# Performance work log

Measured on AMD Instinct MI355X. Metric: run time of the kernel, lower is better.

The kernel has to match this reference:

```python
import jax, jax.numpy as jnp
import numpy as np
from jax import lax

WINDOW = 11
SIGMA = 1.5
K1 = 0.01
K2 = 0.03
DATA_RANGE = 1.0


def _gaussian_kernel(channels):
    coords = jnp.arange(WINDOW, dtype=jnp.float32) - (WINDOW // 2)
    g = jnp.exp(-(coords ** 2) / (2.0 * SIGMA ** 2))
    g = g / g.sum()
    k2d = g[:, None] * g[None, :]                      # [W, W]
    # depthwise kernel, OIHW with I=1, O=channels (feature_group_count=channels)
    return jnp.broadcast_to(k2d, (channels, 1, WINDOW, WINDOW))


def _depthwise_blur(img, kernel, channels):
    pad = WINDOW // 2
    return lax.conv_general_dilated(
        img, kernel,
        window_strides=(1, 1),
        padding=[(pad, pad), (pad, pad)],
        dimension_numbers=('NCHW', 'OIHW', 'NCHW'),
        feature_group_count=channels,
    )


def setup_inputs() -> dict:
    key = jax.random.key(0)
    kx, ky = jax.random.split(key)
    shape = (16, 3, 512, 512)
    x = jax.random.uniform(kx, shape, dtype=jnp.float32)
    y = jax.random.uniform(ky, shape, dtype=jnp.float32)
    return {"x": x, "y": y}


def reference(x, y):
    channels = x.shape[1]
    kernel = _gaussian_kernel(channels)

    mu_x = _depthwise_blur(x, kernel, channels)
    mu_y = _depthwise_blur(y, kernel, channels)
    mu_x_sq = mu_x * mu_x
    mu_y_sq = mu_y * mu_y
    mu_xy = mu_x * mu_y

    sigma_x_sq = _depthwise_blur(x * x, kernel, channels) - mu_x_sq
    sigma_y_sq = _depthwise_blur(y * y, kernel, channels) - mu_y_sq
    sigma_xy = _depthwise_blur(x * y, kernel, channels) - mu_xy

    C1 = (K1 * DATA_RANGE) ** 2
    C2 = (K2 * DATA_RANGE) ** 2
    numerator = (2.0 * mu_xy + C1) * (2.0 * sigma_xy + C2)
    denominator = (mu_x_sq + mu_y_sq + C1) * (sigma_x_sq + sigma_y_sq + C2)
    ssim_map = numerator / (denominator + 1e-8)
    return 1.0 - ssim_map.mean()
```

## Files before the change

kernel.cpp:

```cpp
#include <hip/hip_runtime.h>
#include <cmath>

#define WIN 11
#define HALO 5
#define IMG 512
#define NIMG 48
#define TS 64
#define HR (TS + 2*HALO)
#define NTILE (IMG/TS)
#define NBLK (NIMG*NTILE*NTILE)
#define NPIX (16.0 * 3.0 * 512.0 * 512.0)

typedef _Float16 f16;
typedef _Float16 h2 __attribute__((ext_vector_type(2)));

struct GaussW { float w[WIN]; };

__device__ __forceinline__ unsigned pk2(float a, float b) {
    auto h = __builtin_amdgcn_cvt_pkrtz(a, b);
    return __builtin_bit_cast(unsigned, h);
}
__device__ __forceinline__ h2 uph(unsigned u) {
    return __builtin_bit_cast(h2, u);
}

__global__ void __launch_bounds__(64) zero_kernel(float* out) {
    if (threadIdx.x == 0) out[0] = 0.f;
}

__global__ void __launch_bounds__(64) finish_kernel(float* out) {
    if (threadIdx.x == 0)
        out[0] = 1.0f - out[0] * (float)(1.0 / NPIX);
}

template<int USE_ATOMIC>
__global__ void __launch_bounds__(256) fused_ssim(
        const float* __restrict__ xin, const float* __restrict__ yin,
        float* __restrict__ outp, GaussW W) {
    __shared__ uint4 hb[HR][32];
    __shared__ float wsum[4];
    const int tid = threadIdx.x;
    const int tx = blockIdx.x, ty = blockIdx.y;
    const size_t ibase = (size_t)blockIdx.z * (size_t)(IMG * IMG);
    const float* __restrict__ xb = xin + ibase;
    const float* __restrict__ yb = yin + ibase;

    const int cg  = tid & 15;
    const int rr  = tid >> 4;
    const int gx0 = tx * TS + cg * 4 - HALO;
    const bool cint = (gx0 >= 0) && (gx0 + 13 < IMG);

    #pragma unroll
    for (int it = 0; it < 5; ++it) {
        const int r = it * 16 + rr;
        if (r < HR) {
            const int gy = ty * TS - HALO + r;
            if ((unsigned)gy < IMG) {
                const float* xr = xb + (size_t)gy * IMG;
                const float* yr = yb + (size_t)gy * IMG;
                float xv[14], yv[14];
                if (cint) {
                    xv[0] = xr[gx0];  yv[0] = yr[gx0];
                    #pragma unroll
                    for (int q = 0; q < 3; ++q) {
                        float4 a = *(const float4*)(xr + gx0 + 1 + 4*q);
                        float4 b = *(const float4*)(yr + gx0 + 1 + 4*q);
                        xv[1+4*q]=a.x; xv[2+4*q]=a.y; xv[3+4*q]=a.z; xv[4+4*q]=a.w;
                        yv[1+4*q]=b.x; yv[2+4*q]=b.y; yv[3+4*q]=b.z; yv[4+4*q]=b.w;
                    }
                    xv[13] = xr[gx0 + 13];  yv[13] = yr[gx0 + 13];
                } else {
                    #pragma unroll
                    for (int j = 0; j < 14; ++j) {
                        int gx = gx0 + j;
                        bool ok = ((unsigned)gx < IMG);
                        xv[j] = ok ? xr[gx] : 0.f;
                        yv[j] = ok ? yr[gx] : 0.f;
                    }
                }
                float ax[4]  = {0,0,0,0}, ay[4]  = {0,0,0,0};
                float as_[4] = {0,0,0,0}, axy[4] = {0,0,0,0};
                #pragma unroll
                for (int j = 0; j < 14; ++j) {
                    float xs = xv[j], ys = yv[j];
                    float xy = xs * ys;
                    float ss = fmaf(xs, xs, ys * ys);
                    #pragma unroll
                    for (int o = 0; o < 4; ++o) {
                        int k = j - o;
                        if (k >= 0 && k < WIN) {
                            float wk = W.w[k];
                            ax[o]  += wk * xs;  ay[o]  += wk * ys;
                            as_[o] += wk * ss;  axy[o] += wk * xy;
                        }
                    }
                }
                uint4 u0, u1;
                u0.x = pk2(ax[0],  ax[1]);  u0.y = pk2(ay[0],  ay[1]);
                u0.z = pk2(as_[0], as_[1]); u0.w = pk2(axy[0], axy[1]);
                u1.x = pk2(ax[2],  ax[3]);  u1.y = pk2(ay[2],  ay[3]);
                u1.z = pk2(as_[2], as_[3]); u1.w = pk2(axy[2], axy[3]);
                hb[r][cg]      = u0;
                hb[r][cg + 16] = u1;
            } else {
                uint4 z = make_uint4(0u, 0u, 0u, 0u);
                hb[r][cg]      = z;
                hb[r][cg + 16] = z;
            }
        }
    }
    __syncthreads();

    const int idx = tid & 31;
    const int r0  = (tid >> 5) * 8;

    h2 w2[WIN];
    #pragma unroll
    for (int k = 0; k < WIN; ++k) {
        f16 wk = (f16)W.w[k];
        w2[k] = (h2){wk, wk};
    }

    const float C1 = 0.01f * 0.01f;
    const float C2 = 0.03f * 0.03f;
    float local = 0.f;
    #pragma unroll
    for (int half = 0; half < 2; ++half) {
        const int rbase = r0 + half * 4;
        uint4 v[14];
        #pragma unroll
        for (int j = 0; j < 14; ++j) v[j] = hb[rbase + j][idx];
        #pragma unroll
        for (int o = 0; o < 4; ++o) {
            h2 a0 = (h2){(f16)0,(f16)0}, a1 = a0, a2 = a0, a3 = a0;
            #pragma unroll
            for (int k = 0; k < WIN; ++k) {
                uint4 u = v[o + k];
                h2 wk = w2[k];
                a0 += wk * uph(u.x);
                a1 += wk * uph(u.y);
                a2 += wk * uph(u.z);
                a3 += wk * uph(u.w);
            }
            #pragma unroll
            for (int h = 0; h < 2; ++h) {
                float mux = (float)a0[h];
                float muy = (float)a1[h];
                float es  = (float)a2[h];
                float exy = (float)a3[h];
                float mux2 = mux * mux, muy2 = muy * muy, muxy = mux * muy;
                float num = (2.f * muxy + C1) * (2.f * (exy - muxy) + C2);
                float den = (mux2 + muy2 + C1) * ((es - mux2 - muy2) + C2);
                local += num * __builtin_amdgcn_rcpf(den + 1e-8f);
            }
        }
    }

    #pragma unroll
    for (int off = 32; off > 0; off >>= 1)
        local += __shfl_down(local, off, 64);
    if ((tid & 63) == 0) wsum[tid >> 6] = local;
    __syncthreads();
    if (tid == 0) {
        float bs = wsum[0] + wsum[1] + wsum[2] + wsum[3];
        if (USE_ATOMIC) {
            atomicAdd(outp, bs);
        } else {
            int bid = (blockIdx.z * NTILE + blockIdx.y) * NTILE + blockIdx.x;
            outp[bid] = bs;
        }
    }
}

__global__ void __launch_bounds__(256) reduce_kernel(
        const float* __restrict__ partial, float* __restrict__ out) {
    __shared__ float wsum[4];
    const int tid = threadIdx.x;
    float s = 0.f;
    for (int i = tid; i < NBLK; i += 256) s += partial[i];
    #pragma unroll
    for (int off = 32; off > 0; off >>= 1)
        s += __shfl_down(s, off, 64);
    if ((tid & 63) == 0) wsum[tid >> 6] = s;
    __syncthreads();
    if (tid == 0)
        out[0] = 1.0f - (wsum[0] + wsum[1] + wsum[2] + wsum[3]) * (float)(1.0 / NPIX);
}

extern "C" void kernel_launch(void* const* d_in, const int* in_sizes, int n_in,
                              void* d_out, int out_size, void* d_ws, size_t ws_size,
                              hipStream_t stream) {
    const float* x = (const float*)d_in[0];
    const float* y = (const float*)d_in[1];
    float* out = (float*)d_out;

    GaussW gw;
    double g[WIN], s = 0.0;
    for (int i = 0; i < WIN; ++i) {
        double d = (double)(i - WIN / 2);
        g[i] = exp(-(d * d) / (2.0 * 1.5 * 1.5));
        s += g[i];
    }
    for (int i = 0; i < WIN; ++i) gw.w[i] = (float)(g[i] / s);

    if (ws_size >= (size_t)NBLK * sizeof(float)) {
        float* partial = (float*)d_ws;
        hipLaunchKernelGGL((fused_ssim<0>), dim3(NTILE, NTILE, NIMG), dim3(256),
                           0, stream, x, y, partial, gw);
        hipLaunchKernelGGL(reduce_kernel, dim3(1), dim3(256), 0, stream,
                           partial, out);
    } else {
        hipLaunchKernelGGL(zero_kernel, dim3(1), dim3(64), 0, stream, out);
        hipLaunchKernelGGL((fused_ssim<1>), dim3(NTILE, NTILE, NIMG), dim3(256),
                           0, stream, x, y, out, gw);
        hipLaunchKernelGGL(finish_kernel, dim3(1), dim3(64), 0, stream, out);
    }
}
```

Before: 174.0 us.

## Double block size to 512 threads and stream vertical pass with register accumulators

Raises the block size from 256 to 512 threads per 64x64 tile, so each thread loads fewer halo rows in the horizontal pass and produces 4 output rows instead of 8 in the vertical pass. The vertical blur now streams each shared-memory row once into 16 packed-half accumulators instead of buffering 14 uint4 rows in registers. A launch bound of 512 threads with 8 blocks per CU is set to cut register pressure and raise occupancy. The cost is more threads per tile doing the same halo reads and a larger per-block reduction, plus a risk of register spills under the tighter bound.

```diff
diff --git a/kernel.cpp b/kernel.cpp
--- a/kernel.cpp
+++ b/kernel.cpp
@@ -34,11 +34,11 @@
 }
 
 template<int USE_ATOMIC>
-__global__ void __launch_bounds__(256) fused_ssim(
+__global__ void __launch_bounds__(512, 8) fused_ssim(
         const float* __restrict__ xin, const float* __restrict__ yin,
         float* __restrict__ outp, GaussW W) {
     __shared__ uint4 hb[HR][32];
-    __shared__ float wsum[4];
+    __shared__ float wsum[8];
     const int tid = threadIdx.x;
     const int tx = blockIdx.x, ty = blockIdx.y;
     const size_t ibase = (size_t)blockIdx.z * (size_t)(IMG * IMG);
@@ -51,8 +51,8 @@
     const bool cint = (gx0 >= 0) && (gx0 + 13 < IMG);
 
     #pragma unroll
-    for (int it = 0; it < 5; ++it) {
-        const int r = it * 16 + rr;
+    for (int it = 0; it < 3; ++it) {
+        const int r = it * 32 + rr;
         if (r < HR) {
             const int gy = ty * TS - HALO + r;
             if ((unsigned)gy < IMG) {
@@ -112,7 +112,7 @@
     __syncthreads();
 
     const int idx = tid & 31;
-    const int r0  = (tid >> 5) * 8;
+    const int rbase = (tid >> 5) * 4;
 
     h2 w2[WIN];
     #pragma unroll
@@ -121,38 +121,45 @@
         w2[k] = (h2){wk, wk};
     }
 
+    h2 acc[4][4];
+    #pragma unroll
+    for (int o = 0; o < 4; ++o)
+        #pragma unroll
+        for (int f = 0; f < 4; ++f)
+            acc[o][f] = (h2){(f16)0, (f16)0};
+
+    #pragma unroll
+    for (int j = 0; j < 14; ++j) {
+        uint4 u = hb[rbase + j][idx];
+        h2 f0 = uph(u.x), f1 = uph(u.y), f2 = uph(u.z), f3 = uph(u.w);
+        #pragma unroll
+        for (int o = 0; o < 4; ++o) {
+            int k = j - o;
+            if (k >= 0 && k < WIN) {
+                h2 wk = w2[k];
+                acc[o][0] += wk * f0;
+                acc[o][1] += wk * f1;
+                acc[o][2] += wk * f2;
+                acc[o][3] += wk * f3;
+            }
+        }
+    }
+
     const float C1 = 0.01f * 0.01f;
     const float C2 = 0.03f * 0.03f;
     float local = 0.f;
     #pragma unroll
-    for (int half = 0; half < 2; ++half) {
-        const int rbase = r0 + half * 4;
-        uint4 v[14];
-        #pragma unroll
-        for (int j = 0; j < 14; ++j) v[j] = hb[rbase + j][idx];
-        #pragma unroll
-        for (int o = 0; o < 4; ++o) {
-            h2 a0 = (h2){(f16)0,(f16)0}, a1 = a0, a2 = a0, a3 = a0;
-            #pragma unroll
-            for (int k = 0; k < WIN; ++k) {
-                uint4 u = v[o + k];
-                h2 wk = w2[k];
-                a0 += wk * uph(u.x);
-                a1 += wk * uph(u.y);
-                a2 += wk * uph(u.z);
-                a3 += wk * uph(u.w);
-            }
-            #pragma unroll
-            for (int h = 0; h < 2; ++h) {
-                float mux = (float)a0[h];
-                float muy = (float)a1[h];
-                float es  = (float)a2[h];
-                float exy = (float)a3[h];
-                float mux2 = mux * mux, muy2 = muy * muy, muxy = mux * muy;
-                float num = (2.f * muxy + C1) * (2.f * (exy - muxy) + C2);
-                float den = (mux2 + muy2 + C1) * ((es - mux2 - muy2) + C2);
-                local += num * __builtin_amdgcn_rcpf(den + 1e-8f);
-            }
+    for (int o = 0; o < 4; ++o) {
+        #pragma unroll
+        for (int h = 0; h < 2; ++h) {
+            float mux = (float)acc[o][0][h];
+            float muy = (float)acc[o][1][h];
+            float es  = (float)acc[o][2][h];
+            float exy = (float)acc[o][3][h];
+            float mux2 = mux * mux, muy2 = muy * muy, muxy = mux * muy;
+            float num = (2.f * muxy + C1) * (2.f * (exy - muxy) + C2);
+            float den = (mux2 + muy2 + C1) * ((es - mux2 - muy2) + C2);
+            local += num * __builtin_amdgcn_rcpf(den + 1e-8f);
         }
     }
 
@@ -162,7 +169,9 @@
     if ((tid & 63) == 0) wsum[tid >> 6] = local;
     __syncthreads();
     if (tid == 0) {
-        float bs = wsum[0] + wsum[1] + wsum[2] + wsum[3];
+        float bs = 0.f;
+        #pragma unroll
+        for (int wv = 0; wv < 8; ++wv) bs += wsum[wv];
         if (USE_ATOMIC) {
             atomicAdd(outp, bs);
         } else {
@@ -205,13 +214,13 @@
 
     if (ws_size >= (size_t)NBLK * sizeof(float)) {
         float* partial = (float*)d_ws;
-        hipLaunchKernelGGL((fused_ssim<0>), dim3(NTILE, NTILE, NIMG), dim3(256),
+        hipLaunchKernelGGL((fused_ssim<0>), dim3(NTILE, NTILE, NIMG), dim3(512),
                            0, stream, x, y, partial, gw);
         hipLaunchKernelGGL(reduce_kernel, dim3(1), dim3(256), 0, stream,
                            partial, out);
     } else {
         hipLaunchKernelGGL(zero_kernel, dim3(1), dim3(64), 0, stream, out);
-        hipLaunchKernelGGL((fused_ssim<1>), dim3(NTILE, NTILE, NIMG), dim3(256),
+        hipLaunchKernelGGL((fused_ssim<1>), dim3(NTILE, NTILE, NIMG), dim3(512),
                            0, stream, x, y, out, gw);
         hipLaunchKernelGGL(finish_kernel, dim3(1), dim3(64), 0, stream, out);
     }
```

Result: faster. 165.9 us (-4.7%).
